# Kernel optimization log

Measured on AMD Instinct MI355X. Metric: run time of the kernel, lower is better.

## Reference

```python
import jax, jax.numpy as jnp
import numpy as np

N, E, D, ED, SH = 100000, 1600000, 64, 16, 9

# Real spherical harmonics l=0,1,2, 'integral' normalization (e3nn default),
# applied to unit direction vectors. Coefficients: 1/(2*sqrt(pi)), sqrt(3/4pi), etc.

def _sh(d):
    x, y, z = d[:, 0], d[:, 1], d[:, 2]
    return jnp.stack([
        jnp.full_like(x, 0.28209479177387814),          # l=0
        0.4886025119029199 * y,                          # l=1, m=-1
        0.4886025119029199 * z,                          # l=1, m=0
        0.4886025119029199 * x,                          # l=1, m=1
        1.0925484305920792 * x * y,                      # l=2, m=-2
        1.0925484305920792 * y * z,                      # l=2, m=-1
        0.31539156525252005 * (3.0 * z * z - 1.0),       # l=2, m=0
        1.0925484305920792 * x * z,                      # l=2, m=1
        0.5462742152960396 * (x * x - y * y),            # l=2, m=2
    ], axis=1)


def _mlp(h, W1, b1, W2, b2):  # Linear -> SiLU -> Linear
    return jax.nn.silu(h @ W1 + b1) @ W2 + b2


def setup_inputs() -> dict:
    key = jax.random.key(0)
    ks = jax.random.split(key, 16)
    def rn(k, shape, scale=0.05):
        return jax.random.normal(k, shape, dtype=jnp.float32) * scale
    return {
        "x": jax.random.normal(ks[0], (N, D), jnp.float32),
        "pos": jax.random.normal(ks[1], (N, 3), jnp.float32) * 3.0,
        "edge_attr": jax.random.normal(ks[2], (E, ED), jnp.float32),
        "row": jax.random.randint(ks[3], (E,), 0, N, dtype=jnp.int32),
        "col": jax.random.randint(ks[4], (E,), 0, N, dtype=jnp.int32),
        "node_W1": rn(ks[5], (D, D)), "node_b1": jnp.zeros((D,), jnp.float32),
        "node_W2": rn(ks[6], (D, D)), "node_b2": jnp.zeros((D,), jnp.float32),
        "edge_W1": rn(ks[7], (SH + ED, D)), "edge_b1": jnp.zeros((D,), jnp.float32),
        "edge_W2": rn(ks[8], (D, D)), "edge_b2": jnp.zeros((D,), jnp.float32),
        "out_W1": rn(ks[9], (2 * D, D)), "out_b1": jnp.zeros((D,), jnp.float32),
        "out_W2": rn(ks[10], (D, D)), "out_b2": jnp.zeros((D,), jnp.float32),
        "bn_gamma": jnp.ones((D,), jnp.float32), "bn_beta": jnp.zeros((D,), jnp.float32),
    }


def reference(x, pos, edge_attr, row, col,
              node_W1, node_b1, node_W2, node_b2,
              edge_W1, edge_b1, edge_W2, edge_b2,
              out_W1, out_b1, out_W2, out_b2,
              bn_gamma, bn_beta):
    # gather node positions per edge -> relative vectors
    rel = pos[row] - pos[col]                                    # [E,3]
    length = jnp.sqrt(jnp.sum(rel * rel, axis=1, keepdims=True) + 1e-12)
    d = rel / length
    d = d / (jnp.sqrt(jnp.sum(d * d, axis=1, keepdims=True)) + 1e-10)
    edge_sh = _sh(d)                                             # [E,9]
    edge_feat = jnp.concatenate([edge_sh, edge_attr], axis=1)    # [E,9+ED]
    x_t = _mlp(x, node_W1, node_b1, node_W2, node_b2)            # [N,D]
    e_w = _mlp(edge_feat, edge_W1, edge_b1, edge_W2, edge_b2)    # [E,D]
    msg = x_t[row] * e_w                                         # message = x_j * edge_attr
    # scatter-mean onto target nodes (edge_index[1] == col)
    s = jax.ops.segment_sum(msg, col, num_segments=N)            # [N,D]
    cnt = jax.ops.segment_sum(jnp.ones((E,), msg.dtype), col, num_segments=N)
    agg = s / jnp.maximum(cnt, 1.0)[:, None]
    h = jnp.concatenate([agg, x], axis=1)                        # [N,2D]
    h = _mlp(h, out_W1, out_b1, out_W2, out_b2)                  # [N,D]
    # BatchNorm over node dim (scalar irreps), training-mode batch stats
    mean = jnp.mean(h, axis=0)
    var = jnp.var(h, axis=0)
    return (h - mean) / jnp.sqrt(var + 1e-5) * bn_gamma + bn_beta
```

## Files before the change

### kernel.cpp

```cpp
#include <hip/hip_runtime.h>
#include <math.h>

#define DD 64
#define EDA 16

#define FR_E1 0
#define FR_E2 4
#define FR_N1 12
#define FR_N2 20
#define FR_O1 28
#define FR_O2 44
#define FR_TOT 52

#define PADH 72
#define PADF 68

#define HS 72
#define MS 136

typedef unsigned int u32;
typedef unsigned long long u64;
typedef __attribute__((ext_vector_type(8))) short short8;
typedef __attribute__((ext_vector_type(4))) float f32x4;

static __device__ __forceinline__ float silu(float v) {
    return v / (1.0f + __expf(-v));
}
static __device__ __forceinline__ unsigned short f2bf(float f) {
    unsigned u = __float_as_uint(f);
    unsigned r = u + 0x7FFFu + ((u >> 16) & 1u);
    return (unsigned short)(r >> 16);
}
static __device__ __forceinline__ float bf2f(unsigned short u) {
    return __uint_as_float(((unsigned)u) << 16);
}
static __device__ __forceinline__ unsigned cvt_pk_bf16(float lo, float hi) {
    unsigned r;
    asm("v_cvt_pk_bf16_f32 %0, %1, %2" : "=v"(r) : "v"(lo), "v"(hi));
    return r;
}
static __device__ __forceinline__ int bperm(int idx_lane, int v) {
    return __builtin_amdgcn_ds_bpermute(idx_lane << 2, v);
}
static __device__ __forceinline__ void wave_lds_fence() {
    asm volatile("s_waitcnt lgkmcnt(0)" ::: "memory");
    __builtin_amdgcn_sched_barrier(0);
}

__global__ __launch_bounds__(256) void k_pack_w(
    const float* __restrict__ eW1, const float* __restrict__ eW2,
    const float* __restrict__ nW1, const float* __restrict__ nW2,
    const float* __restrict__ oW1, const float* __restrict__ oW2,
    unsigned short* __restrict__ wpk)
{
    int t = threadIdx.x;
    int nt = t >> 6, l = t & 63;
    int kc = l >> 4, n0 = l & 15;

    #pragma unroll
    for (int j = 0; j < 8; ++j) {
        int k = kc*8 + j;
        int orig = (k < 16) ? (9 + k) : ((k < 25) ? (k - 16) : -1);
        float v = (orig >= 0) ? eW1[orig*DD + nt*16 + n0] : 0.0f;
        wpk[((size_t)((FR_E1 + nt)*64 + l))*8 + j] = f2bf(v);
    }
    #pragma unroll
    for (int s = 0; s < 2; ++s) {
        #pragma unroll
        for (int j = 0; j < 8; ++j) {
            int k = s*32 + kc*8 + j;
            wpk[((size_t)((FR_E2 + s*4 + nt)*64 + l))*8 + j] = f2bf(eW2[k*DD + nt*16 + n0]);
            wpk[((size_t)((FR_N1 + s*4 + nt)*64 + l))*8 + j] = f2bf(nW1[k*DD + nt*16 + n0]);
            wpk[((size_t)((FR_N2 + s*4 + nt)*64 + l))*8 + j] = f2bf(nW2[k*DD + nt*16 + n0]);
            wpk[((size_t)((FR_O2 + s*4 + nt)*64 + l))*8 + j] = f2bf(oW2[k*DD + nt*16 + n0]);
        }
    }
    #pragma unroll
    for (int s = 0; s < 4; ++s) {
        #pragma unroll
        for (int j = 0; j < 8; ++j) {
            int k = s*32 + kc*8 + j;
            wpk[((size_t)((FR_O1 + s*4 + nt)*64 + l))*8 + j] = f2bf(oW1[k*DD + nt*16 + n0]);
        }
    }
}

__global__ __launch_bounds__(256, 2) void k_node_hist(
    const float* __restrict__ x,
    const unsigned short* __restrict__ wpk,
    const float* __restrict__ b1, const float* __restrict__ b2,
    unsigned short* __restrict__ x_tb, int n, int nodeBlocks,
    const int* __restrict__ col, u32* __restrict__ cnt, int n_e)
{
    __shared__ __align__(16) unsigned short tile[4][16*PADH];
    const int tid  = threadIdx.x;

    if (blockIdx.x >= nodeBlocks) {
        int g = (blockIdx.x - nodeBlocks) * 256 + tid;
        int base = g * 4;
        if (base + 3 < n_e) {
            int4 c = ((const int4*)col)[g];
            atomicAdd(&cnt[c.x], 1u);
            atomicAdd(&cnt[c.y], 1u);
            atomicAdd(&cnt[c.z], 1u);
            atomicAdd(&cnt[c.w], 1u);
        } else {
            for (int e = base; e < n_e; ++e) atomicAdd(&cnt[col[e]], 1u);
        }
        return;
    }

    const int wv   = tid >> 6;
    const int lane = tid & 63;
    const int kc   = lane >> 4;
    const int n0   = lane & 15;
    const int rbase = kc * 4;

    const short8* fb = (const short8*)wpk;
    short8 bw1[2][4], bw2[2][4];
    #pragma unroll
    for (int s = 0; s < 2; ++s)
        #pragma unroll
        for (int nt = 0; nt < 4; ++nt) {
            bw1[s][nt] = fb[(FR_N1 + s*4 + nt)*64 + lane];
            bw2[s][nt] = fb[(FR_N2 + s*4 + nt)*64 + lane];
        }
    float b1v[4], b2v[4];
    #pragma unroll
    for (int nt = 0; nt < 4; ++nt) { b1v[nt] = b1[nt*16 + n0]; b2v[nt] = b2[nt*16 + n0]; }

    const int base = blockIdx.x*64 + wv*16;
    int rc = min(base + n0, n - 1);
    const float* xr = x + (size_t)rc * DD;

    short8 a[2];
    #pragma unroll
    for (int m = 0; m < 2; ++m) {
        float4 u0 = *(const float4*)(xr + m*32 + kc*8);
        float4 u1 = *(const float4*)(xr + m*32 + kc*8 + 4);
        unsigned* au = (unsigned*)&a[m];
        au[0] = cvt_pk_bf16(u0.x, u0.y);
        au[1] = cvt_pk_bf16(u0.z, u0.w);
        au[2] = cvt_pk_bf16(u1.x, u1.y);
        au[3] = cvt_pk_bf16(u1.z, u1.w);
    }

    f32x4 zz = {0.f, 0.f, 0.f, 0.f};
    f32x4 hacc[4] = {zz, zz, zz, zz};
    #pragma unroll
    for (int m = 0; m < 2; ++m)
        #pragma unroll
        for (int nt = 0; nt < 4; ++nt)
            hacc[nt] = __builtin_amdgcn_mfma_f32_16x16x32_bf16(a[m], bw1[m][nt], hacc[nt], 0, 0, 0);

    #pragma unroll
    for (int nt = 0; nt < 4; ++nt)
        #pragma unroll
        for (int r = 0; r < 4; ++r)
            tile[wv][(rbase + r)*PADH + nt*16 + n0] = f2bf(silu(hacc[nt][r] + b1v[nt]));
    __syncthreads();

    short8 a2_0 = *(const short8*)&tile[wv][n0*PADH +  0 + kc*8];
    short8 a2_1 = *(const short8*)&tile[wv][n0*PADH + 32 + kc*8];
    f32x4 oacc[4];
    #pragma unroll
    for (int nt = 0; nt < 4; ++nt) {
        oacc[nt] = __builtin_amdgcn_mfma_f32_16x16x32_bf16(a2_0, bw2[0][nt], zz, 0, 0, 0);
        oacc[nt] = __builtin_amdgcn_mfma_f32_16x16x32_bf16(a2_1, bw2[1][nt], oacc[nt], 0, 0, 0);
    }
    __syncthreads();

    #pragma unroll
    for (int nt = 0; nt < 4; ++nt)
        #pragma unroll
        for (int r = 0; r < 4; ++r)
            tile[wv][(rbase + r)*PADH + nt*16 + n0] = f2bf(oacc[nt][r] + b2v[nt]);
    __syncthreads();

    int ei = lane >> 2, q = lane & 3;
    int er = base + ei;
    if (er < n) {
        uint4* dst = (uint4*)(x_tb + (size_t)er * DD);
        dst[q]     = *(const uint4*)&tile[wv][ei*PADH + q*8];
        dst[q + 4] = *(const uint4*)&tile[wv][ei*PADH + (q + 4)*8];
    }
}

__global__ __launch_bounds__(256) void k_scan1(
    const u32* __restrict__ cnt, u32* __restrict__ bsum, int n)
{
    __shared__ u32 s[256];
    int i = blockIdx.x * 256 + threadIdx.x;
    s[threadIdx.x] = (i < n) ? cnt[i] : 0u;
    __syncthreads();
    for (int o = 128; o > 0; o >>= 1) {
        if (threadIdx.x < o) s[threadIdx.x] += s[threadIdx.x + o];
        __syncthreads();
    }
    if (threadIdx.x == 0) bsum[blockIdx.x] = s[0];
}

__global__ __launch_bounds__(512) void k_scan2(
    const u32* __restrict__ bsum, u32* __restrict__ boff, int nb)
{
    __shared__ u32 s[512];
    int t = threadIdx.x;
    u32 v = (t < nb) ? bsum[t] : 0u;
    s[t] = v;
    __syncthreads();
    for (int o = 1; o < 512; o <<= 1) {
        u32 a = (t >= o) ? s[t - o] : 0u;
        __syncthreads();
        s[t] += a;
        __syncthreads();
    }
    if (t < nb) boff[t] = s[t] - v;
}

__global__ __launch_bounds__(256) void k_scan3(
    const u32* __restrict__ cnt, const u32* __restrict__ boff,
    u32* __restrict__ wp, int n)
{
    __shared__ u32 s[256];
    int t = threadIdx.x;
    int i = blockIdx.x * 256 + t;
    u32 v = (i < n) ? cnt[i] : 0u;
    s[t] = v;
    __syncthreads();
    for (int o = 1; o < 256; o <<= 1) {
        u32 a = (t >= o) ? s[t - o] : 0u;
        __syncthreads();
        s[t] += a;
        __syncthreads();
    }
    if (i < n) wp[i] = boff[blockIdx.x] + s[t] - v;
}

__global__ __launch_bounds__(256) void k_scatter(
    const int* __restrict__ row, const int* __restrict__ col,
    u32* __restrict__ wp, u64* __restrict__ ce,
    float* __restrict__ agg, int n_agg4, int n_e)
{
    int e = blockIdx.x * 256 + threadIdx.x;
    if (e < n_agg4) {
        float4 z = {0.f, 0.f, 0.f, 0.f};
        ((float4*)agg)[e] = z;
    }
    if (e >= n_e) return;
    int c = col[e];
    int r = row[e];
    u32 p = atomicAdd(&wp[c], 1u);
    u32 lo = (u32)e | ((u32)r << 21);
    u32 hi = ((u32)r >> 11) | ((u32)c << 6);
    u64 pk = (u64)lo | ((u64)hi << 32);
    __builtin_nontemporal_store(pk, &ce[p]);
}

__global__ __launch_bounds__(256, 3) void k_edge_fused(
    const float* __restrict__ pos,
    const float* __restrict__ edge_attr,
    const u64* __restrict__ ce,
    const unsigned short* __restrict__ x_tb,
    const unsigned short* __restrict__ wpk,
    const float* __restrict__ b1, const float* __restrict__ b2,
    float* __restrict__ agg, int n_e)
{
    __shared__ __align__(16) unsigned short hid_s[4][16*HS];
    __shared__ __align__(16) unsigned short msg_s[4][16*MS];

    const int tid  = threadIdx.x;
    const int wv   = tid >> 6;
    const int lane = tid & 63;
    const int kc   = lane >> 4;
    const int n0   = lane & 15;

    const short8* fb = (const short8*)wpk;
    short8 bw1[4], bw2[2][4];
    #pragma unroll
    for (int nt = 0; nt < 4; ++nt) bw1[nt] = fb[(FR_E1 + nt)*64 + lane];
    #pragma unroll
    for (int s = 0; s < 2; ++s)
        #pragma unroll
        for (int nt = 0; nt < 4; ++nt) bw2[s][nt] = fb[(FR_E2 + s*4 + nt)*64 + lane];

    float4 b1q[4], b2q[4];
    #pragma unroll
    for (int nt = 0; nt < 4; ++nt) {
        b1q[nt] = *(const float4*)(b1 + nt*16 + kc*4);
        b2q[nt] = *(const float4*)(b2 + nt*16 + kc*4);
    }

    const int gbase = blockIdx.x*256 + wv*64;
    int g  = gbase + lane;
    int gc = min(g, n_e - 1);
    u64 pk = ce[gc];
    u32 pklo = (u32)pk, pkhi = (u32)(pk >> 32);
    int eo = (int)(pklo & 0x1FFFFFu);
    int rw = (int)((pklo >> 21) | ((pkhi & 0x3Fu) << 11));
    int cl = (int)(pkhi >> 6);

    float ax = pos[3*rw+0] - pos[3*cl+0];
    float ay = pos[3*rw+1] - pos[3*cl+1];
    float az = pos[3*rw+2] - pos[3*cl+2];
    float len = sqrtf(fmaf(ax,ax, fmaf(ay,ay, az*az)) + 1e-12f);
    float dx = ax/len, dy = ay/len, dz = az/len;
    float n2 = sqrtf(fmaf(dx,dx, fmaf(dy,dy, dz*dz)));
    float inv = 1.0f/(n2 + 1e-10f);
    dx *= inv; dy *= inv; dz *= inv;

    u32 shp01 = cvt_pk_bf16(0.28209479177387814f, 0.4886025119029199f*dy);
    u32 shp23 = cvt_pk_bf16(0.4886025119029199f*dz, 0.4886025119029199f*dx);
    u32 shp45 = cvt_pk_bf16(1.0925484305920792f*dx*dy, 1.0925484305920792f*dy*dz);
    u32 shp67 = cvt_pk_bf16(0.31539156525252005f*(3.0f*dz*dz - 1.0f),
                            1.0925484305920792f*dx*dz);
    u32 shp8  = cvt_pk_bf16(0.5462742152960396f*(dx*dx - dy*dy), 0.0f);

    int cln = bperm(min(lane + 1, 63), cl);
    u64 fmask = __ballot(cln != cl) | 0x8000800080008000ull;

    f32x4 zz = {0.f, 0.f, 0.f, 0.f};

    int    Prv;
    float4 Pa0, Pa1;
    uint2  Px0, Px1, Px2, Px3;
    u32    Ps01, Ps23, Ps45, Ps67, Ps8;

    auto ISSUE = [&](int tt) {
        const int le = tt*16 + n0;
        int ea = bperm(le, eo);
        Prv    = bperm(le, rw);
        Ps01 = (u32)bperm(le, (int)shp01);
        Ps23 = (u32)bperm(le, (int)shp23);
        Ps45 = (u32)bperm(le, (int)shp45);
        Ps67 = (u32)bperm(le, (int)shp67);
        Ps8  = (u32)bperm(le, (int)shp8);
        if (kc < 2) {
            const float4* ap = (const float4*)(edge_attr + (size_t)ea*EDA + kc*8);
            Pa0 = ap[0];
            Pa1 = ap[1];
        }
        const unsigned short* xrow = x_tb + (size_t)Prv * DD;
        Px0 = *(const uint2*)(xrow +  0 + kc*4);
        Px1 = *(const uint2*)(xrow + 16 + kc*4);
        Px2 = *(const uint2*)(xrow + 32 + kc*4);
        Px3 = *(const uint2*)(xrow + 48 + kc*4);
    };

    ISSUE(0);

    #pragma unroll
    for (int tt = 0; tt < 4; ++tt) {
        float4 a0 = Pa0, a1 = Pa1;
        uint2 xv0 = Px0, xv1 = Px1, xv2 = Px2, xv3 = Px3;
        u32 s01 = Ps01, s23 = Ps23, s45 = Ps45, s67 = Ps67, s8 = Ps8;
        if (tt < 3) ISSUE(tt + 1);

        bool valid = (gbase + tt*16 + n0) < n_e;

        short8 af;
        unsigned* au = (unsigned*)&af;
        if (kc < 2) {
            au[0] = cvt_pk_bf16(a0.x, a0.y);
            au[1] = cvt_pk_bf16(a0.z, a0.w);
            au[2] = cvt_pk_bf16(a1.x, a1.y);
            au[3] = cvt_pk_bf16(a1.z, a1.w);
        } else if (kc == 2) {
            au[0] = s01; au[1] = s23; au[2] = s45; au[3] = s67;
        } else {
            au[0] = s8; au[1] = 0u; au[2] = 0u; au[3] = 0u;
        }

        f32x4 hacc[4];
        #pragma unroll
        for (int nt = 0; nt < 4; ++nt)
            hacc[nt] = __builtin_amdgcn_mfma_f32_16x16x32_bf16(bw1[nt], af, zz, 0, 0, 0);

        #pragma unroll
        for (int nt = 0; nt < 4; ++nt) {
            float h0 = silu(hacc[nt][0] + b1q[nt].x);
            float h1 = silu(hacc[nt][1] + b1q[nt].y);
            float h2 = silu(hacc[nt][2] + b1q[nt].z);
            float h3 = silu(hacc[nt][3] + b1q[nt].w);
            uint2 pr;
            pr.x = cvt_pk_bf16(h0, h1);
            pr.y = cvt_pk_bf16(h2, h3);
            *(uint2*)&hid_s[wv][n0*HS + nt*16 + kc*4] = pr;
        }
        wave_lds_fence();

        short8 bf0 = *(const short8*)&hid_s[wv][n0*HS +  0 + kc*8];
        short8 bf1 = *(const short8*)&hid_s[wv][n0*HS + 32 + kc*8];
        f32x4 oacc[4];
        #pragma unroll
        for (int nt = 0; nt < 4; ++nt) {
            oacc[nt] = __builtin_amdgcn_mfma_f32_16x16x32_bf16(bw2[0][nt], bf0, zz, 0, 0, 0);
            oacc[nt] = __builtin_amdgcn_mfma_f32_16x16x32_bf16(bw2[1][nt], bf1, oacc[nt], 0, 0, 0);
        }

        if (!valid) {
            xv0.x = xv0.y = xv1.x = xv1.y = 0u;
            xv2.x = xv2.y = xv3.x = xv3.y = 0u;
        }
        {
            float m0, m1, m2, m3;
            uint2 pr;
            m0 = (oacc[0][0] + b2q[0].x) * bf2f((unsigned short)(xv0.x));
            m1 = (oacc[0][1] + b2q[0].y) * bf2f((unsigned short)(xv0.x >> 16));
            m2 = (oacc[0][2] + b2q[0].z) * bf2f((unsigned short)(xv0.y));
            m3 = (oacc[0][3] + b2q[0].w) * bf2f((unsigned short)(xv0.y >> 16));
            pr.x = cvt_pk_bf16(m0, m1); pr.y = cvt_pk_bf16(m2, m3);
            *(uint2*)&msg_s[wv][n0*MS +  0 + kc*4] = pr;
            m0 = (oacc[1][0] + b2q[1].x) * bf2f((unsigned short)(xv1.x));
            m1 = (oacc[1][1] + b2q[1].y) * bf2f((unsigned short)(xv1.x >> 16));
            m2 = (oacc[1][2] + b2q[1].z) * bf2f((unsigned short)(xv1.y));
            m3 = (oacc[1][3] + b2q[1].w) * bf2f((unsigned short)(xv1.y >> 16));
            pr.x = cvt_pk_bf16(m0, m1); pr.y = cvt_pk_bf16(m2, m3);
            *(uint2*)&msg_s[wv][n0*MS + 16 + kc*4] = pr;
            m0 = (oacc[2][0] + b2q[2].x) * bf2f((unsigned short)(xv2.x));
            m1 = (oacc[2][1] + b2q[2].y) * bf2f((unsigned short)(xv2.x >> 16));
            m2 = (oacc[2][2] + b2q[2].z) * bf2f((unsigned short)(xv2.y));
            m3 = (oacc[2][3] + b2q[2].w) * bf2f((unsigned short)(xv2.y >> 16));
            pr.x = cvt_pk_bf16(m0, m1); pr.y = cvt_pk_bf16(m2, m3);
            *(uint2*)&msg_s[wv][n0*MS + 32 + kc*4] = pr;
            m0 = (oacc[3][0] + b2q[3].x) * bf2f((unsigned short)(xv3.x));
            m1 = (oacc[3][1] + b2q[3].y) * bf2f((unsigned short)(xv3.x >> 16));
            m2 = (oacc[3][2] + b2q[3].z) * bf2f((unsigned short)(xv3.y));
            m3 = (oacc[3][3] + b2q[3].w) * bf2f((unsigned short)(xv3.y >> 16));
            pr.x = cvt_pk_bf16(m0, m1); pr.y = cvt_pk_bf16(m2, m3);
            *(uint2*)&msg_s[wv][n0*MS + 48 + kc*4] = pr;
        }
        wave_lds_fence();

        {
            float acc = 0.0f;
            #pragma unroll
            for (int r = 0; r < 16; ++r) {
                acc += bf2f(msg_s[wv][r*MS + lane]);
                if ((fmask >> (tt*16 + r)) & 1ull) {
                    int cur = __builtin_amdgcn_readlane(cl, tt*16 + r);
                    unsafeAtomicAdd(&agg[(size_t)cur*DD + lane], acc);
                    acc = 0.0f;
                }
            }
        }
    }
}

__global__ __launch_bounds__(256, 2) void k_out_mfma(
    const float* __restrict__ agg, const u32* __restrict__ cnt,
    const float* __restrict__ x,
    const unsigned short* __restrict__ wpk,
    const float* __restrict__ b1, const float* __restrict__ b2,
    float* __restrict__ h, float* __restrict__ sums, int n)
{
    __shared__ __align__(16) unsigned short htile[4][16*PADH];
    __shared__ __align__(16) float otile[4][16*PADF];
    const int tid  = threadIdx.x;
    const int wv   = tid >> 6;
    const int lane = tid & 63;
    const int kc   = lane >> 4;
    const int n0   = lane & 15;
    const int rbase = kc * 4;

    const short8* fb = (const short8*)wpk;
    short8 bw1[4][4], bw2[2][4];
    #pragma unroll
    for (int s = 0; s < 4; ++s)
        #pragma unroll
        for (int nt = 0; nt < 4; ++nt) bw1[s][nt] = fb[(FR_O1 + s*4 + nt)*64 + lane];
    #pragma unroll
    for (int s = 0; s < 2; ++s)
        #pragma unroll
        for (int nt = 0; nt < 4; ++nt) bw2[s][nt] = fb[(FR_O2 + s*4 + nt)*64 + lane];

    float b1v[4], b2v[4];
    #pragma unroll
    for (int nt = 0; nt < 4; ++nt) { b1v[nt] = b1[nt*16 + n0]; b2v[nt] = b2[nt*16 + n0]; }

    const int base = blockIdx.x*64 + wv*16;
    int rc = min(base + n0, n - 1);
    const float* ar = agg + (size_t)rc * DD;
    const float* xr = x   + (size_t)rc * DD;
    float invc = 1.0f / fmaxf((float)cnt[rc], 1.0f);

    short8 a[4];
    #pragma unroll
    for (int m = 0; m < 4; ++m) {
        const float* src = (m < 2) ? (ar + m*32 + kc*8) : (xr + (m-2)*32 + kc*8);
        float4 u0 = *(const float4*)(src);
        float4 u1 = *(const float4*)(src + 4);
        if (m < 2) {
            u0.x*=invc; u0.y*=invc; u0.z*=invc; u0.w*=invc;
            u1.x*=invc; u1.y*=invc; u1.z*=invc; u1.w*=invc;
        }
        unsigned* au = (unsigned*)&a[m];
        au[0] = cvt_pk_bf16(u0.x, u0.y);
        au[1] = cvt_pk_bf16(u0.z, u0.w);
        au[2] = cvt_pk_bf16(u1.x, u1.y);
        au[3] = cvt_pk_bf16(u1.z, u1.w);
    }

    f32x4 zz = {0.f, 0.f, 0.f, 0.f};
    f32x4 hacc[4] = {zz, zz, zz, zz};
    #pragma unroll
    for (int m = 0; m < 4; ++m)
        #pragma unroll
        for (int nt = 0; nt < 4; ++nt)
            hacc[nt] = __builtin_amdgcn_mfma_f32_16x16x32_bf16(a[m], bw1[m][nt], hacc[nt], 0, 0, 0);

    #pragma unroll
    for (int nt = 0; nt < 4; ++nt)
        #pragma unroll
        for (int r = 0; r < 4; ++r)
            htile[wv][(rbase + r)*PADH + nt*16 + n0] = f2bf(silu(hacc[nt][r] + b1v[nt]));
    __syncthreads();

    short8 a2_0 = *(const short8*)&htile[wv][n0*PADH +  0 + kc*8];
    short8 a2_1 = *(const short8*)&htile[wv][n0*PADH + 32 + kc*8];
    f32x4 oacc[4];
    #pragma unroll
    for (int nt = 0; nt < 4; ++nt) {
        oacc[nt] = __builtin_amdgcn_mfma_f32_16x16x32_bf16(a2_0, bw2[0][nt], zz, 0, 0, 0);
        oacc[nt] = __builtin_amdgcn_mfma_f32_16x16x32_bf16(a2_1, bw2[1][nt], oacc[nt], 0, 0, 0);
    }

    #pragma unroll
    for (int nt = 0; nt < 4; ++nt)
        #pragma unroll
        for (int r = 0; r < 4; ++r)
            otile[wv][(rbase + r)*PADF + nt*16 + n0] = oacc[nt][r] + b2v[nt];
    __syncthreads();

    int ei = lane >> 2, q = lane & 3;
    int er = base + ei;
    if (er < n) {
        float4* dst = (float4*)(h + (size_t)er * DD);
        #pragma unroll
        for (int k = 0; k < 4; ++k)
            dst[q + 4*k] = *(const float4*)&otile[wv][ei*PADF + (q + 4*k)*4];
    }

    if (tid < 64) {
        int f = tid;
        float s = 0.f, qq = 0.f;
        #pragma unroll
        for (int w = 0; w < 4; ++w) {
            int base_w = blockIdx.x*64 + w*16;
            int nv = n - base_w;
            nv = nv < 0 ? 0 : (nv > 16 ? 16 : nv);
            for (int r = 0; r < nv; ++r) {
                float v = otile[w][r*PADF + f];
                s += v; qq = fmaf(v, v, qq);
            }
        }
        unsafeAtomicAdd(&sums[f], s);
        unsafeAtomicAdd(&sums[DD + f], qq);
    }
}

__global__ __launch_bounds__(256) void k_bn_norm(
    float* __restrict__ h, const float* __restrict__ sums,
    const float* __restrict__ gamma, const float* __restrict__ beta,
    float inv_n, int total4)
{
    int g = blockIdx.x*256 + threadIdx.x;
    if (g >= total4) return;
    int f0 = (g*4) & (DD-1);
    float4 v = ((const float4*)h)[g];
    float4 sm = *(const float4*)(sums + f0);
    float4 sq = *(const float4*)(sums + DD + f0);
    float4 gm = *(const float4*)(gamma + f0);
    float4 bt = *(const float4*)(beta + f0);
    float m0 = sm.x*inv_n, m1 = sm.y*inv_n, m2 = sm.z*inv_n, m3 = sm.w*inv_n;
    float s0 = gm.x * rsqrtf(sq.x*inv_n - m0*m0 + 1e-5f);
    float s1 = gm.y * rsqrtf(sq.y*inv_n - m1*m1 + 1e-5f);
    float s2 = gm.z * rsqrtf(sq.z*inv_n - m2*m2 + 1e-5f);
    float s3 = gm.w * rsqrtf(sq.w*inv_n - m3*m3 + 1e-5f);
    v.x = fmaf(v.x - m0, s0, bt.x);
    v.y = fmaf(v.y - m1, s1, bt.y);
    v.z = fmaf(v.z - m2, s2, bt.z);
    v.w = fmaf(v.w - m3, s3, bt.w);
    ((float4*)h)[g] = v;
}

static inline size_t al16(size_t v) { return (v + 15) & ~(size_t)15; }

extern "C" void kernel_launch(void* const* d_in, const int* in_sizes, int n_in,
                              void* d_out, int out_size, void* d_ws, size_t ws_size,
                              hipStream_t stream)
{
    const float* x         = (const float*)d_in[0];
    const float* pos       = (const float*)d_in[1];
    const float* edge_attr = (const float*)d_in[2];
    const int*   row       = (const int*)d_in[3];
    const int*   col       = (const int*)d_in[4];
    const float* nW1 = (const float*)d_in[5];
    const float* nb1 = (const float*)d_in[6];
    const float* nW2 = (const float*)d_in[7];
    const float* nb2 = (const float*)d_in[8];
    const float* eW1 = (const float*)d_in[9];
    const float* eb1 = (const float*)d_in[10];
    const float* eW2 = (const float*)d_in[11];
    const float* eb2 = (const float*)d_in[12];
    const float* oW1 = (const float*)d_in[13];
    const float* ob1 = (const float*)d_in[14];
    const float* oW2 = (const float*)d_in[15];
    const float* ob2 = (const float*)d_in[16];
    const float* gamma = (const float*)d_in[17];
    const float* beta  = (const float*)d_in[18];

    const int N = in_sizes[0] / DD;
    const int E = in_sizes[3];
    const int NB = (N + 255) / 256;
    const int nodeBlocks = (N + 63) / 64;
    const int histBlocks = (E/4 + 255) / 256;

    float* hout = (float*)d_out;
    char* ws = (char*)d_ws;

    size_t o_xtb  = 0;
    size_t o_cnt  = o_xtb  + (size_t)N*DD*2;
    size_t o_sums = o_cnt  + (size_t)N*4;
    size_t o_agg  = o_sums + 128*4;
    size_t o_wp   = o_agg  + (size_t)N*DD*4;
    size_t o_bsum = o_wp   + (size_t)N*4;
    size_t o_boff = al16(o_bsum + (size_t)NB*4);
    size_t o_wpk  = al16(o_boff + (size_t)NB*4);
    size_t o_ce   = al16(o_wpk + (size_t)FR_TOT*64*8*2);
    size_t need   = o_ce + (size_t)E*8;

    if (ws_size < need) return;

    unsigned short* x_tb = (unsigned short*)(ws + o_xtb);
    u32*   cnt  = (u32*)(ws + o_cnt);
    float* sums = (float*)(ws + o_sums);
    float* agg  = (float*)(ws + o_agg);
    u32*   wp   = (u32*)(ws + o_wp);
    u32*   bsum = (u32*)(ws + o_bsum);
    u32*   boff = (u32*)(ws + o_boff);
    unsigned short* wpk = (unsigned short*)(ws + o_wpk);
    u64*   ce   = (u64*)(ws + o_ce);

    hipMemsetAsync(cnt, 0, (size_t)N*4 + 128*4, stream);

    k_pack_w<<<1, 256, 0, stream>>>(eW1, eW2, nW1, nW2, oW1, oW2, wpk);
    k_node_hist<<<nodeBlocks + histBlocks, 256, 0, stream>>>(
        x, wpk, nb1, nb2, x_tb, N, nodeBlocks, col, cnt, E);
    k_scan1<<<NB, 256, 0, stream>>>(cnt, bsum, N);
    k_scan2<<<1, 512, 0, stream>>>(bsum, boff, NB);
    k_scan3<<<NB, 256, 0, stream>>>(cnt, boff, wp, N);
    k_scatter<<<(E + 255)/256, 256, 0, stream>>>(row, col, wp, ce, agg, N*DD/4, E);
    k_edge_fused<<<(E + 255)/256, 256, 0, stream>>>(pos, edge_attr, ce, x_tb,
                                                    wpk, eb1, eb2, agg, E);
    k_out_mfma<<<(N + 63)/64, 256, 0, stream>>>(agg, cnt, x, wpk, ob1, ob2, hout, sums, N);
    k_bn_norm<<<(N*DD/4 + 255)/256, 256, 0, stream>>>(hout, sums, gamma, beta,
                                                      1.0f/(float)N, N*DD/4);
}
```

Measured before the change: 335.9 us.

## Raise edge-kernel occupancy by moving W2 fragments to LDS and dropping prefetch

The edge kernel's launch bound rises from 3 to 8 blocks per SM. To fit that register budget, the second-layer weight fragments are staged once per block into shared memory and read from there, instead of being held in registers. Both bias vectors are packed to bf16 pairs, and the hidden and message tiles share one LDS buffer. The explicit software prefetch of the next tile's gathers is replaced by a non-unrolled loop, so more resident waves hide gather latency instead. The cost is extra LDS reads per MFMA, a block barrier at startup, and slightly lower bias precision.

```diff
diff --git a/kernel.cpp b/kernel.cpp
--- a/kernel.cpp
+++ b/kernel.cpp
@@ -16,7 +16,6 @@
 #define PADF 68
 
 #define HS 72
-#define MS 136
 
 typedef unsigned int u32;
 typedef unsigned long long u64;
@@ -33,6 +32,12 @@
 }
 static __device__ __forceinline__ float bf2f(unsigned short u) {
     return __uint_as_float(((unsigned)u) << 16);
+}
+static __device__ __forceinline__ float bflo(u32 v) {
+    return __uint_as_float(v << 16);
+}
+static __device__ __forceinline__ float bfhi(u32 v) {
+    return __uint_as_float(v & 0xFFFF0000u);
 }
 static __device__ __forceinline__ unsigned cvt_pk_bf16(float lo, float hi) {
     unsigned r;
@@ -256,7 +261,7 @@
     __builtin_nontemporal_store(pk, &ce[p]);
 }
 
-__global__ __launch_bounds__(256, 3) void k_edge_fused(
+__global__ __launch_bounds__(256, 8) void k_edge_fused(
     const float* __restrict__ pos,
     const float* __restrict__ edge_attr,
     const u64* __restrict__ ce,
@@ -265,8 +270,8 @@
     const float* __restrict__ b1, const float* __restrict__ b2,
     float* __restrict__ agg, int n_e)
 {
-    __shared__ __align__(16) unsigned short hid_s[4][16*HS];
-    __shared__ __align__(16) unsigned short msg_s[4][16*MS];
+    __shared__ __align__(16) unsigned short t_s[4][16*HS];
+    __shared__ __align__(16) unsigned short wls[8*64*8];
 
     const int tid  = threadIdx.x;
     const int wv   = tid >> 6;
@@ -274,20 +279,25 @@
     const int kc   = lane >> 4;
     const int n0   = lane & 15;
 
+    {
+        const uint4* wsrc = (const uint4*)(wpk + FR_E2*64*8);
+        uint4* wdst = (uint4*)wls;
+        wdst[tid*2]     = wsrc[tid*2];
+        wdst[tid*2 + 1] = wsrc[tid*2 + 1];
+    }
+
     const short8* fb = (const short8*)wpk;
-    short8 bw1[4], bw2[2][4];
+    short8 bw1[4];
     #pragma unroll
     for (int nt = 0; nt < 4; ++nt) bw1[nt] = fb[(FR_E1 + nt)*64 + lane];
-    #pragma unroll
-    for (int s = 0; s < 2; ++s)
-        #pragma unroll
-        for (int nt = 0; nt < 4; ++nt) bw2[s][nt] = fb[(FR_E2 + s*4 + nt)*64 + lane];
-
-    float4 b1q[4], b2q[4];
+
+    uint2 bp1[4], bp2[4];
     #pragma unroll
     for (int nt = 0; nt < 4; ++nt) {
-        b1q[nt] = *(const float4*)(b1 + nt*16 + kc*4);
-        b2q[nt] = *(const float4*)(b2 + nt*16 + kc*4);
+        float4 q1 = *(const float4*)(b1 + nt*16 + kc*4);
+        float4 q2 = *(const float4*)(b2 + nt*16 + kc*4);
+        bp1[nt].x = cvt_pk_bf16(q1.x, q1.y); bp1[nt].y = cvt_pk_bf16(q1.z, q1.w);
+        bp2[nt].x = cvt_pk_bf16(q2.x, q2.y); bp2[nt].y = cvt_pk_bf16(q2.z, q2.w);
     }
 
     const int gbase = blockIdx.x*256 + wv*64;
@@ -320,46 +330,32 @@
 
     f32x4 zz = {0.f, 0.f, 0.f, 0.f};
 
-    int    Prv;
-    float4 Pa0, Pa1;
-    uint2  Px0, Px1, Px2, Px3;
-    u32    Ps01, Ps23, Ps45, Ps67, Ps8;
-
-    auto ISSUE = [&](int tt) {
+    __syncthreads();
+
+    #pragma unroll 1
+    for (int tt = 0; tt < 4; ++tt) {
         const int le = tt*16 + n0;
-        int ea = bperm(le, eo);
-        Prv    = bperm(le, rw);
-        Ps01 = (u32)bperm(le, (int)shp01);
-        Ps23 = (u32)bperm(le, (int)shp23);
-        Ps45 = (u32)bperm(le, (int)shp45);
-        Ps67 = (u32)bperm(le, (int)shp67);
-        Ps8  = (u32)bperm(le, (int)shp8);
-        if (kc < 2) {
-            const float4* ap = (const float4*)(edge_attr + (size_t)ea*EDA + kc*8);
-            Pa0 = ap[0];
-            Pa1 = ap[1];
-        }
-        const unsigned short* xrow = x_tb + (size_t)Prv * DD;
-        Px0 = *(const uint2*)(xrow +  0 + kc*4);
-        Px1 = *(const uint2*)(xrow + 16 + kc*4);
-        Px2 = *(const uint2*)(xrow + 32 + kc*4);
-        Px3 = *(const uint2*)(xrow + 48 + kc*4);
-    };
-
-    ISSUE(0);
-
-    #pragma unroll
-    for (int tt = 0; tt < 4; ++tt) {
-        float4 a0 = Pa0, a1 = Pa1;
-        uint2 xv0 = Px0, xv1 = Px1, xv2 = Px2, xv3 = Px3;
-        u32 s01 = Ps01, s23 = Ps23, s45 = Ps45, s67 = Ps67, s8 = Ps8;
-        if (tt < 3) ISSUE(tt + 1);
-
-        bool valid = (gbase + tt*16 + n0) < n_e;
+        bool valid = (gbase + le) < n_e;
+
+        int ea  = bperm(le, eo);
+        int rv  = bperm(le, rw);
+        u32 s01 = (u32)bperm(le, (int)shp01);
+        u32 s23 = (u32)bperm(le, (int)shp23);
+        u32 s45 = (u32)bperm(le, (int)shp45);
+        u32 s67 = (u32)bperm(le, (int)shp67);
+        u32 s8  = (u32)bperm(le, (int)shp8);
+
+        const unsigned short* xrow = x_tb + (size_t)rv * DD;
+        uint2 xv0 = *(const uint2*)(xrow +  0 + kc*4);
+        uint2 xv1 = *(const uint2*)(xrow + 16 + kc*4);
+        uint2 xv2 = *(const uint2*)(xrow + 32 + kc*4);
+        uint2 xv3 = *(const uint2*)(xrow + 48 + kc*4);
 
         short8 af;
         unsigned* au = (unsigned*)&af;
         if (kc < 2) {
+            const float4* ap = (const float4*)(edge_attr + (size_t)ea*EDA + kc*8);
+            float4 a0 = ap[0], a1 = ap[1];
             au[0] = cvt_pk_bf16(a0.x, a0.y);
             au[1] = cvt_pk_bf16(a0.z, a0.w);
             au[2] = cvt_pk_bf16(a1.x, a1.y);
@@ -377,24 +373,26 @@
 
         #pragma unroll
         for (int nt = 0; nt < 4; ++nt) {
-            float h0 = silu(hacc[nt][0] + b1q[nt].x);
-            float h1 = silu(hacc[nt][1] + b1q[nt].y);
-            float h2 = silu(hacc[nt][2] + b1q[nt].z);
-            float h3 = silu(hacc[nt][3] + b1q[nt].w);
+            float h0 = silu(hacc[nt][0] + bflo(bp1[nt].x));
+            float h1 = silu(hacc[nt][1] + bfhi(bp1[nt].x));
+            float h2 = silu(hacc[nt][2] + bflo(bp1[nt].y));
+            float h3 = silu(hacc[nt][3] + bfhi(bp1[nt].y));
             uint2 pr;
             pr.x = cvt_pk_bf16(h0, h1);
             pr.y = cvt_pk_bf16(h2, h3);
-            *(uint2*)&hid_s[wv][n0*HS + nt*16 + kc*4] = pr;
+            *(uint2*)&t_s[wv][n0*HS + nt*16 + kc*4] = pr;
         }
         wave_lds_fence();
 
-        short8 bf0 = *(const short8*)&hid_s[wv][n0*HS +  0 + kc*8];
-        short8 bf1 = *(const short8*)&hid_s[wv][n0*HS + 32 + kc*8];
+        short8 bf0 = *(const short8*)&t_s[wv][n0*HS +  0 + kc*8];
+        short8 bf1 = *(const short8*)&t_s[wv][n0*HS + 32 + kc*8];
         f32x4 oacc[4];
         #pragma unroll
         for (int nt = 0; nt < 4; ++nt) {
-            oacc[nt] = __builtin_amdgcn_mfma_f32_16x16x32_bf16(bw2[0][nt], bf0, zz, 0, 0, 0);
-            oacc[nt] = __builtin_amdgcn_mfma_f32_16x16x32_bf16(bw2[1][nt], bf1, oacc[nt], 0, 0, 0);
+            short8 w0 = *(const short8*)&wls[((0*4 + nt)*64 + lane)*8];
+            oacc[nt] = __builtin_amdgcn_mfma_f32_16x16x32_bf16(w0, bf0, zz, 0, 0, 0);
+            short8 w1 = *(const short8*)&wls[((1*4 + nt)*64 + lane)*8];
+            oacc[nt] = __builtin_amdgcn_mfma_f32_16x16x32_bf16(w1, bf1, oacc[nt], 0, 0, 0);
         }
 
         if (!valid) {
@@ -404,30 +402,30 @@
         {
             float m0, m1, m2, m3;
             uint2 pr;
-            m0 = (oacc[0][0] + b2q[0].x) * bf2f((unsigned short)(xv0.x));
-            m1 = (oacc[0][1] + b2q[0].y) * bf2f((unsigned short)(xv0.x >> 16));
-            m2 = (oacc[0][2] + b2q[0].z) * bf2f((unsigned short)(xv0.y));
-            m3 = (oacc[0][3] + b2q[0].w) * bf2f((unsigned short)(xv0.y >> 16));
+            m0 = (oacc[0][0] + bflo(bp2[0].x)) * bflo(xv0.x);
+            m1 = (oacc[0][1] + bfhi(bp2[0].x)) * bfhi(xv0.x);
+            m2 = (oacc[0][2] + bflo(bp2[0].y)) * bflo(xv0.y);
+            m3 = (oacc[0][3] + bfhi(bp2[0].y)) * bfhi(xv0.y);
             pr.x = cvt_pk_bf16(m0, m1); pr.y = cvt_pk_bf16(m2, m3);
-            *(uint2*)&msg_s[wv][n0*MS +  0 + kc*4] = pr;
-            m0 = (oacc[1][0] + b2q[1].x) * bf2f((unsigned short)(xv1.x));
-            m1 = (oacc[1][1] + b2q[1].y) * bf2f((unsigned short)(xv1.x >> 16));
-            m2 = (oacc[1][2] + b2q[1].z) * bf2f((unsigned short)(xv1.y));
-            m3 = (oacc[1][3] + b2q[1].w) * bf2f((unsigned short)(xv1.y >> 16));
+            *(uint2*)&t_s[wv][n0*HS +  0 + kc*4] = pr;
+            m0 = (oacc[1][0] + bflo(bp2[1].x)) * bflo(xv1.x);
+            m1 = (oacc[1][1] + bfhi(bp2[1].x)) * bfhi(xv1.x);
+            m2 = (oacc[1][2] + bflo(bp2[1].y)) * bflo(xv1.y);
+            m3 = (oacc[1][3] + bfhi(bp2[1].y)) * bfhi(xv1.y);
             pr.x = cvt_pk_bf16(m0, m1); pr.y = cvt_pk_bf16(m2, m3);
-            *(uint2*)&msg_s[wv][n0*MS + 16 + kc*4] = pr;
-            m0 = (oacc[2][0] + b2q[2].x) * bf2f((unsigned short)(xv2.x));
-            m1 = (oacc[2][1] + b2q[2].y) * bf2f((unsigned short)(xv2.x >> 16));
-            m2 = (oacc[2][2] + b2q[2].z) * bf2f((unsigned short)(xv2.y));
-            m3 = (oacc[2][3] + b2q[2].w) * bf2f((unsigned short)(xv2.y >> 16));
+            *(uint2*)&t_s[wv][n0*HS + 16 + kc*4] = pr;
+            m0 = (oacc[2][0] + bflo(bp2[2].x)) * bflo(xv2.x);
+            m1 = (oacc[2][1] + bfhi(bp2[2].x)) * bfhi(xv2.x);
+            m2 = (oacc[2][2] + bflo(bp2[2].y)) * bflo(xv2.y);
+            m3 = (oacc[2][3] + bfhi(bp2[2].y)) * bfhi(xv2.y);
             pr.x = cvt_pk_bf16(m0, m1); pr.y = cvt_pk_bf16(m2, m3);
-            *(uint2*)&msg_s[wv][n0*MS + 32 + kc*4] = pr;
-            m0 = (oacc[3][0] + b2q[3].x) * bf2f((unsigned short)(xv3.x));
-            m1 = (oacc[3][1] + b2q[3].y) * bf2f((unsigned short)(xv3.x >> 16));
-            m2 = (oacc[3][2] + b2q[3].z) * bf2f((unsigned short)(xv3.y));
-            m3 = (oacc[3][3] + b2q[3].w) * bf2f((unsigned short)(xv3.y >> 16));
+            *(uint2*)&t_s[wv][n0*HS + 32 + kc*4] = pr;
+            m0 = (oacc[3][0] + bflo(bp2[3].x)) * bflo(xv3.x);
+            m1 = (oacc[3][1] + bfhi(bp2[3].x)) * bfhi(xv3.x);
+            m2 = (oacc[3][2] + bflo(bp2[3].y)) * bflo(xv3.y);
+            m3 = (oacc[3][3] + bfhi(bp2[3].y)) * bfhi(xv3.y);
             pr.x = cvt_pk_bf16(m0, m1); pr.y = cvt_pk_bf16(m2, m3);
-            *(uint2*)&msg_s[wv][n0*MS + 48 + kc*4] = pr;
+            *(uint2*)&t_s[wv][n0*HS + 48 + kc*4] = pr;
         }
         wave_lds_fence();
 
@@ -435,7 +433,7 @@
             float acc = 0.0f;
             #pragma unroll
             for (int r = 0; r < 16; ++r) {
-                acc += bf2f(msg_s[wv][r*MS + lane]);
+                acc += bf2f(t_s[wv][r*HS + lane]);
                 if ((fmask >> (tt*16 + r)) & 1ull) {
                     int cur = __builtin_amdgcn_readlane(cl, tt*16 + r);
                     unsafeAtomicAdd(&agg[(size_t)cur*DD + lane], acc);
```

Result: slower. 502.1 us (+49.5%).
